# Kernel tuning notes

Hardware: AMD Instinct MI355X
Metric: run time of the kernel (lower is better)

Reference implementation:

```python
import jax, jax.numpy as jnp
import numpy as np

N = 100_000   # nodes
E = 1_600_000 # edges
G, H1, H2, Z = 64, 64, 64, 32


def _w(k, o, i):
    return jax.random.normal(k, (o, i), jnp.float32) * (1.0 / np.sqrt(i))


def setup_inputs() -> dict:
    key = jax.random.key(0)
    ks = jax.random.split(key, 16)
    inp = {
        "x": jax.random.normal(ks[0], (N, G), jnp.float32),
        "edge_src": jax.random.randint(ks[1], (E,), 0, N, jnp.int32),
        "edge_dst": jax.random.randint(ks[2], (E,), 0, N, jnp.int32),
        "eps": jax.random.normal(ks[3], (N, Z), jnp.float32),
        "W1": _w(ks[4], H1, G),  "b1": jnp.zeros((H1,), jnp.float32),
        "W2": _w(ks[5], H2, H1), "b2": jnp.zeros((H2,), jnp.float32),
        "W31": _w(ks[6], Z, H2), "b31": jnp.zeros((Z,), jnp.float32),
        "W32": _w(ks[7], Z, H2), "b32": jnp.zeros((Z,), jnp.float32),
        "W4": _w(ks[8], H2, Z),  "b4": jnp.zeros((H2,), jnp.float32),
        "W5": _w(ks[9], H1, H2), "b5": jnp.zeros((H1,), jnp.float32),
        "W6": _w(ks[10], G, H1), "b6": jnp.zeros((G,), jnp.float32),
    }
    return inp


def _gcn(h, W, b, act, src, dst, norm):
    # message: h_src * norm_src, gathered per edge  [E, d]
    m = (h * norm)[src]
    # reduce: sum over incoming edges, scaled by norm_dst  [N, d]
    agg = jax.ops.segment_sum(m, dst, num_segments=N) * norm
    # node apply: linear + activation
    return act(agg @ W.T + b)


def reference(x, edge_src, edge_dst, eps,
              W1, b1, W2, b2, W31, b31, W32, b32, W4, b4, W5, b5, W6, b6):
    # symmetric GCN norm: deg^{-1/2} from in-degree
    deg = jax.ops.segment_sum(jnp.ones((E,), jnp.float32), edge_dst, num_segments=N)
    norm = jax.lax.rsqrt(jnp.maximum(deg, 1.0))[:, None]  # [N,1]

    relu = jax.nn.relu
    ident = lambda h: h

    h = _gcn(x, W1, b1, relu, edge_src, edge_dst, norm)
    h = _gcn(h, W2, b2, relu, edge_src, edge_dst, norm)
    mu = _gcn(h, W31, b31, ident, edge_src, edge_dst, norm)
    log_var = _gcn(h, W32, b32, ident, edge_src, edge_dst, norm)

    z = eps * jnp.exp(0.5 * log_var) + mu

    h = _gcn(z, W4, b4, relu, edge_src, edge_dst, norm)
    h = _gcn(h, W5, b5, relu, edge_src, edge_dst, norm)
    recon = _gcn(h, W6, b6, jax.nn.sigmoid, edge_src, edge_dst, norm)
    return recon, mu, log_var
```

## Files before the change

kernel.cpp:

```cpp
#include <hip/hip_runtime.h>
#include <hip/hip_fp16.h>
#include <math.h>

#define NN 100000
#define NE 1600000
#define NBKT 391
#define CHUNK 8192
#define NB1 ((NE + CHUNK - 1) / CHUNK)

__global__ __launch_bounds__(256) void p0_hist_kernel(const int* __restrict__ dst,
                                                      int* __restrict__ bcnt) {
    __shared__ int h[NBKT];
    for (int b = threadIdx.x; b < NBKT; b += 256) h[b] = 0;
    __syncthreads();
    int e0 = blockIdx.x * CHUNK;
    for (int k = 0; k < CHUNK / 256; ++k) {
        int e = e0 + threadIdx.x + k * 256;
        if (e < NE) atomicAdd(&h[dst[e] >> 8], 1);
    }
    __syncthreads();
    for (int b = threadIdx.x; b < NBKT; b += 256)
        if (h[b]) atomicAdd(&bcnt[b], h[b]);
}

__global__ void scan_buckets_kernel(const int* __restrict__ bcnt, int* __restrict__ bbase,
                                    int* __restrict__ bcur) {
    __shared__ int s[512];
    int tid = threadIdx.x;
    int v = (tid < NBKT) ? bcnt[tid] : 0;
    s[tid] = v;
    __syncthreads();
    for (int off = 1; off < 512; off <<= 1) {
        int t = (tid >= off) ? s[tid - off] : 0;
        __syncthreads();
        s[tid] += t;
        __syncthreads();
    }
    if (tid < NBKT) { int ex = s[tid] - v; bbase[tid] = ex; bcur[tid] = ex; }
    if (tid == NBKT) bbase[NBKT] = NE;
}

__global__ __launch_bounds__(256) void p1_scatter_kernel(const int* __restrict__ src,
                                                         const int* __restrict__ dst,
                                                         int* __restrict__ bcur,
                                                         int2* __restrict__ gpair) {
    __shared__ int h[NBKT], rb[NBKT], hc[NBKT];
    int tid = threadIdx.x;
    for (int b = tid; b < NBKT; b += 256) { h[b] = 0; hc[b] = 0; }
    __syncthreads();
    int e0 = blockIdx.x * CHUNK;
    for (int k = 0; k < CHUNK / 256; ++k) {
        int e = e0 + tid + k * 256;
        if (e < NE) atomicAdd(&h[dst[e] >> 8], 1);
    }
    __syncthreads();
    for (int b = tid; b < NBKT; b += 256)
        rb[b] = h[b] ? atomicAdd(&bcur[b], h[b]) : 0;
    __syncthreads();
    for (int k = 0; k < CHUNK / 256; ++k) {
        int e = e0 + tid + k * 256;
        if (e < NE) {
            int d = dst[e], s = src[e];
            int b = d >> 8;
            int pos = rb[b] + atomicAdd(&hc[b], 1);
            gpair[pos] = make_int2(s, d);
        }
    }
}

__global__ __launch_bounds__(256) void p2_place_kernel(const int2* __restrict__ gpair,
                                                       const int* __restrict__ bbase,
                                                       int* __restrict__ csr,
                                                       int* __restrict__ row_start,
                                                       float* __restrict__ nrm) {
    __shared__ int cnt[256], nexcl[256], pcnt[256];
    int b = blockIdx.x, tid = threadIdx.x;
    int s0 = bbase[b], s1 = bbase[b + 1];
    cnt[tid] = 0; pcnt[tid] = 0;
    __syncthreads();
    for (int i = s0 + tid; i < s1; i += 256)
        atomicAdd(&cnt[gpair[i].y & 255], 1);
    __syncthreads();
    int v = cnt[tid];
    nexcl[tid] = v;
    __syncthreads();
    for (int off = 1; off < 256; off <<= 1) {
        int t = (tid >= off) ? nexcl[tid - off] : 0;
        __syncthreads();
        nexcl[tid] += t;
        __syncthreads();
    }
    int ex = nexcl[tid] - v;
    int node = (b << 8) + tid;
    if (node < NN) {
        row_start[node] = s0 + ex;
        nrm[node] = rsqrtf(fmaxf((float)v, 1.0f));
    }
    if (b == NBKT - 1 && tid == 0) row_start[NN] = NE;
    nexcl[tid] = s0 + ex;
    __syncthreads();
    for (int i = s0 + tid; i < s1; i += 256) {
        int2 p = gpair[i];
        int l = p.y & 255;
        int pos = nexcl[l] + atomicAdd(&pcnt[l], 1);
        csr[pos] = p.x;
    }
}

union H4 { uint2 u; __half2 h[2]; };

__global__ void scale_x_h_kernel(const float4* __restrict__ x4, const float* __restrict__ nrm,
                                 uint2* __restrict__ xs, int total4) {
    int i = blockIdx.x * blockDim.x + threadIdx.x;
    if (i < total4) {
        float nv = nrm[i >> 4];
        float4 v = x4[i];
        H4 w;
        w.h[0] = __floats2half2_rn(v.x * nv, v.y * nv);
        w.h[1] = __floats2half2_rn(v.z * nv, v.w * nv);
        xs[i] = w.u;
    }
}

template<int IN, int ACT, bool SCALE, bool DUAL>
__global__ __launch_bounds__(256) void gcn_fused_kernel(
        const __half* __restrict__ h,
        const float* __restrict__ nrm,
        const int* __restrict__ row_start,
        const int* __restrict__ csr,
        const float* __restrict__ Wa, const float* __restrict__ ba,
        const float* __restrict__ Wb, const float* __restrict__ bb,
        void* __restrict__ outv, float* __restrict__ out2,
        const float* __restrict__ eps, __half* __restrict__ zbuf) {
    __shared__ float Wt[64 * 65];
    __shared__ float bs[64];
    __shared__ __align__(16) float aggS[4][4][IN];

    int tid = threadIdx.x;
    if (DUAL) {
        for (int i = tid; i < 32 * 64; i += 256) {
            int o = i >> 6, k = i & 63;
            Wt[k * 65 + o]      = Wa[i];
            Wt[k * 65 + o + 32] = Wb[i];
        }
        if (tid < 32) { bs[tid] = ba[tid]; bs[tid + 32] = bb[tid]; }
    } else {
        for (int i = tid; i < 64 * IN; i += 256) {
            int o = i / IN, k = i % IN;
            Wt[k * 65 + o] = Wa[i];
        }
        if (tid < 64) bs[tid] = ba[tid];
    }
    __syncthreads();

    constexpr int RL  = IN / 4;
    constexpr int EPI = 64 / RL;
    int wave = tid >> 6, lane = tid & 63;
    int row_slot = lane / RL;
    int f4 = lane % RL;
    int nodeBase = (blockIdx.x * 4 + wave) * 4;

    const uint2* hp = (const uint2*)h;

    int rs[4], re[4];
#pragma unroll
    for (int i = 0; i < 4; ++i) {
        rs[i] = row_start[nodeBase + i];
        re[i] = row_start[nodeBase + i + 1];
    }
    int maxd = max(max(re[0] - rs[0], re[1] - rs[1]), max(re[2] - rs[2], re[3] - rs[3]));

    float4 acc[4];
#pragma unroll
    for (int i = 0; i < 4; ++i) acc[i] = make_float4(0.f, 0.f, 0.f, 0.f);

    for (int t = 0; t < maxd; t += EPI) {
#pragma unroll
        for (int i = 0; i < 4; ++i) {
            int jj = rs[i] + t + row_slot;
            bool ok = jj < re[i];
            int s = csr[ok ? jj : 0];
            float m = ok ? 1.f : 0.f;
            H4 v; v.u = hp[(size_t)s * RL + f4];
            float2 f01 = __half22float2(v.h[0]);
            float2 f23 = __half22float2(v.h[1]);
            acc[i].x = fmaf(m, f01.x, acc[i].x);
            acc[i].y = fmaf(m, f01.y, acc[i].y);
            acc[i].z = fmaf(m, f23.x, acc[i].z);
            acc[i].w = fmaf(m, f23.y, acc[i].w);
        }
    }

#pragma unroll
    for (int i = 0; i < 4; ++i) {
        for (int o = RL; o < 64; o <<= 1) {
            acc[i].x += __shfl_xor(acc[i].x, o);
            acc[i].y += __shfl_xor(acc[i].y, o);
            acc[i].z += __shfl_xor(acc[i].z, o);
            acc[i].w += __shfl_xor(acc[i].w, o);
        }
    }

    if (row_slot == 0) {
#pragma unroll
        for (int i = 0; i < 4; ++i)
            ((float4*)aggS[wave][i])[f4] = acc[i];
    }

#pragma unroll
    for (int i = 0; i < 4; ++i) {
        int node = nodeBase + i;
        float oa = 0.f;
#pragma unroll
        for (int k = 0; k < IN; ++k)
            oa = fmaf(aggS[wave][i][k], Wt[k * 65 + lane], oa);
        float nv = nrm[node];
        oa = oa * nv + bs[lane];
        if (ACT == 1) oa = fmaxf(oa, 0.f);
        if (ACT == 2) oa = 1.f / (1.f + expf(-oa));

        if (DUAL) {
            float* mu_p = (float*)outv;
            if (lane < 32) mu_p[(size_t)node * 32 + lane]        = oa;
            else           out2[(size_t)node * 32 + (lane - 32)] = oa;
            float lv_v = __shfl(oa, (lane + 32) & 63);
            if (lane < 32) {
                float e = eps[(size_t)node * 32 + lane];
                zbuf[(size_t)node * 32 + lane] = __float2half((e * expf(0.5f * lv_v) + oa) * nv);
            }
        } else if (SCALE) {
            ((__half*)outv)[(size_t)node * 64 + lane] = __float2half(oa * nv);
        } else {
            ((float*)outv)[(size_t)node * 64 + lane] = oa;
        }
    }
}

extern "C" void kernel_launch(void* const* d_in, const int* in_sizes, int n_in,
                              void* d_out, int out_size, void* d_ws, size_t ws_size,
                              hipStream_t stream) {
    const float* x    = (const float*)d_in[0];
    const int*   esrc = (const int*)d_in[1];
    const int*   edst = (const int*)d_in[2];
    const float* eps  = (const float*)d_in[3];
    const float* W1  = (const float*)d_in[4];  const float* b1  = (const float*)d_in[5];
    const float* W2  = (const float*)d_in[6];  const float* b2  = (const float*)d_in[7];
    const float* W31 = (const float*)d_in[8];  const float* b31 = (const float*)d_in[9];
    const float* W32 = (const float*)d_in[10]; const float* b32 = (const float*)d_in[11];
    const float* W4  = (const float*)d_in[12]; const float* b4  = (const float*)d_in[13];
    const float* W5  = (const float*)d_in[14]; const float* b5  = (const float*)d_in[15];
    const float* W6  = (const float*)d_in[16]; const float* b6  = (const float*)d_in[17];

    float* outp  = (float*)d_out;
    float* recon = outp;
    float* mu    = outp + (size_t)NN * 64;
    float* lv    = mu   + (size_t)NN * 32;

    int* wsI       = (int*)d_ws;
    int* bcnt      = wsI;
    int* bbase     = bcnt + 392;
    int* bcur      = bbase + 392;
    int* row_start = bcur + 392;
    int* csr       = row_start + NN + 4;
    float* nrm     = (float*)(csr + NE);
    __half* hA     = (__half*)(nrm + NN);
    __half* hB     = hA + (size_t)NN * 64;
    int2* gpair    = (int2*)hA;

    const int SB = 256;
    const int fgrid = NN / 16;

    hipMemsetAsync(bcnt, 0, 392 * sizeof(int), stream);
    p0_hist_kernel<<<NB1, 256, 0, stream>>>(edst, bcnt);
    scan_buckets_kernel<<<1, 512, 0, stream>>>(bcnt, bbase, bcur);
    p1_scatter_kernel<<<NB1, 256, 0, stream>>>(esrc, edst, bcur, gpair);
    p2_place_kernel<<<NBKT, 256, 0, stream>>>(gpair, bbase, csr, row_start, nrm);

    scale_x_h_kernel<<<(NN * 16 + SB - 1) / SB, SB, 0, stream>>>((const float4*)x, nrm, (uint2*)hA, NN * 16);

    gcn_fused_kernel<64, 1, true,  false><<<fgrid, 256, 0, stream>>>(hA, nrm, row_start, csr, W1,  b1,  nullptr, nullptr, hB,    nullptr, nullptr, nullptr);
    gcn_fused_kernel<64, 1, true,  false><<<fgrid, 256, 0, stream>>>(hB, nrm, row_start, csr, W2,  b2,  nullptr, nullptr, hA,    nullptr, nullptr, nullptr);
    gcn_fused_kernel<64, 0, false, true ><<<fgrid, 256, 0, stream>>>(hA, nrm, row_start, csr, W31, b31, W32,     b32,     mu,    lv,      eps,     hB);
    gcn_fused_kernel<32, 1, true,  false><<<fgrid, 256, 0, stream>>>(hB, nrm, row_start, csr, W4,  b4,  nullptr, nullptr, hA,    nullptr, nullptr, nullptr);
    gcn_fused_kernel<64, 1, true,  false><<<fgrid, 256, 0, stream>>>(hA, nrm, row_start, csr, W5,  b5,  nullptr, nullptr, hB,    nullptr, nullptr, nullptr);
    gcn_fused_kernel<64, 2, false, false><<<fgrid, 256, 0, stream>>>(hB, nrm, row_start, csr, W6,  b6,  nullptr, nullptr, recon, nullptr, nullptr, nullptr);
}
```

Baseline: 620.8 us.

## Pack edge pairs into one int and process 8 nodes per wave

The CSR build now packs each (src, dst-low-byte) pair into a single 32-bit int instead of an int2, halving the intermediate scatter traffic. The fused GCN kernel handles 8 nodes per wave instead of 4 and splits the gather loop into separate phases for index loads, feature loads and accumulation, so more independent loads are in flight. The grid is halved to match. The cost is more registers and possible lower occupancy, and a wave now loops to the maximum degree over 8 nodes, which adds masked work.

```diff
diff --git a/kernel.cpp b/kernel.cpp
--- a/kernel.cpp
+++ b/kernel.cpp
@@ -43,7 +43,7 @@
 __global__ __launch_bounds__(256) void p1_scatter_kernel(const int* __restrict__ src,
                                                          const int* __restrict__ dst,
                                                          int* __restrict__ bcur,
-                                                         int2* __restrict__ gpair) {
+                                                         int* __restrict__ gpair) {
     __shared__ int h[NBKT], rb[NBKT], hc[NBKT];
     int tid = threadIdx.x;
     for (int b = tid; b < NBKT; b += 256) { h[b] = 0; hc[b] = 0; }
@@ -63,12 +63,12 @@
             int d = dst[e], s = src[e];
             int b = d >> 8;
             int pos = rb[b] + atomicAdd(&hc[b], 1);
-            gpair[pos] = make_int2(s, d);
-        }
-    }
-}
-
-__global__ __launch_bounds__(256) void p2_place_kernel(const int2* __restrict__ gpair,
+            gpair[pos] = (s << 8) | (d & 255);
+        }
+    }
+}
+
+__global__ __launch_bounds__(256) void p2_place_kernel(const int* __restrict__ gpair,
                                                        const int* __restrict__ bbase,
                                                        int* __restrict__ csr,
                                                        int* __restrict__ row_start,
@@ -79,7 +79,7 @@
     cnt[tid] = 0; pcnt[tid] = 0;
     __syncthreads();
     for (int i = s0 + tid; i < s1; i += 256)
-        atomicAdd(&cnt[gpair[i].y & 255], 1);
+        atomicAdd(&cnt[gpair[i] & 255], 1);
     __syncthreads();
     int v = cnt[tid];
     nexcl[tid] = v;
@@ -100,10 +100,10 @@
     nexcl[tid] = s0 + ex;
     __syncthreads();
     for (int i = s0 + tid; i < s1; i += 256) {
-        int2 p = gpair[i];
-        int l = p.y & 255;
+        int p = gpair[i];
+        int l = p & 255;
         int pos = nexcl[l] + atomicAdd(&pcnt[l], 1);
-        csr[pos] = p.x;
+        csr[pos] = p >> 8;
     }
 }
 
@@ -132,9 +132,10 @@
         const float* __restrict__ Wb, const float* __restrict__ bb,
         void* __restrict__ outv, float* __restrict__ out2,
         const float* __restrict__ eps, __half* __restrict__ zbuf) {
+    constexpr int MLP = 8;
     __shared__ float Wt[64 * 65];
     __shared__ float bs[64];
-    __shared__ __align__(16) float aggS[4][4][IN];
+    __shared__ __align__(16) float aggS[4][MLP][IN];
 
     int tid = threadIdx.x;
     if (DUAL) {
@@ -158,41 +159,52 @@
     int wave = tid >> 6, lane = tid & 63;
     int row_slot = lane / RL;
     int f4 = lane % RL;
-    int nodeBase = (blockIdx.x * 4 + wave) * 4;
+    int nodeBase = (blockIdx.x * 4 + wave) * MLP;
 
     const uint2* hp = (const uint2*)h;
 
-    int rs[4], re[4];
-#pragma unroll
-    for (int i = 0; i < 4; ++i) {
-        rs[i] = row_start[nodeBase + i];
-        re[i] = row_start[nodeBase + i + 1];
-    }
-    int maxd = max(max(re[0] - rs[0], re[1] - rs[1]), max(re[2] - rs[2], re[3] - rs[3]));
-
-    float4 acc[4];
-#pragma unroll
-    for (int i = 0; i < 4; ++i) acc[i] = make_float4(0.f, 0.f, 0.f, 0.f);
+    int rsb[MLP], re[MLP];
+#pragma unroll
+    for (int i = 0; i < MLP; ++i) {
+        rsb[i] = row_start[nodeBase + i];
+        re[i]  = row_start[nodeBase + i + 1];
+    }
+    int maxd = 0;
+#pragma unroll
+    for (int i = 0; i < MLP; ++i) maxd = max(maxd, re[i] - rsb[i]);
+#pragma unroll
+    for (int i = 0; i < MLP; ++i) rsb[i] += row_slot;
+
+    float4 acc[MLP];
+#pragma unroll
+    for (int i = 0; i < MLP; ++i) acc[i] = make_float4(0.f, 0.f, 0.f, 0.f);
 
     for (int t = 0; t < maxd; t += EPI) {
-#pragma unroll
-        for (int i = 0; i < 4; ++i) {
-            int jj = rs[i] + t + row_slot;
+        int s[MLP]; float m[MLP];
+#pragma unroll
+        for (int i = 0; i < MLP; ++i) {
+            int jj = rsb[i] + t;
             bool ok = jj < re[i];
-            int s = csr[ok ? jj : 0];
-            float m = ok ? 1.f : 0.f;
-            H4 v; v.u = hp[(size_t)s * RL + f4];
-            float2 f01 = __half22float2(v.h[0]);
-            float2 f23 = __half22float2(v.h[1]);
-            acc[i].x = fmaf(m, f01.x, acc[i].x);
-            acc[i].y = fmaf(m, f01.y, acc[i].y);
-            acc[i].z = fmaf(m, f23.x, acc[i].z);
-            acc[i].w = fmaf(m, f23.y, acc[i].w);
-        }
-    }
-
-#pragma unroll
-    for (int i = 0; i < 4; ++i) {
+            s[i] = csr[ok ? jj : 0];
+            m[i] = ok ? 1.f : 0.f;
+        }
+        H4 v[MLP];
+#pragma unroll
+        for (int i = 0; i < MLP; ++i)
+            v[i].u = hp[(size_t)s[i] * RL + f4];
+#pragma unroll
+        for (int i = 0; i < MLP; ++i) {
+            float2 f01 = __half22float2(v[i].h[0]);
+            float2 f23 = __half22float2(v[i].h[1]);
+            acc[i].x = fmaf(m[i], f01.x, acc[i].x);
+            acc[i].y = fmaf(m[i], f01.y, acc[i].y);
+            acc[i].z = fmaf(m[i], f23.x, acc[i].z);
+            acc[i].w = fmaf(m[i], f23.y, acc[i].w);
+        }
+    }
+
+#pragma unroll
+    for (int i = 0; i < MLP; ++i) {
         for (int o = RL; o < 64; o <<= 1) {
             acc[i].x += __shfl_xor(acc[i].x, o);
             acc[i].y += __shfl_xor(acc[i].y, o);
@@ -203,12 +215,12 @@
 
     if (row_slot == 0) {
 #pragma unroll
-        for (int i = 0; i < 4; ++i)
+        for (int i = 0; i < MLP; ++i)
             ((float4*)aggS[wave][i])[f4] = acc[i];
     }
 
 #pragma unroll
-    for (int i = 0; i < 4; ++i) {
+    for (int i = 0; i < MLP; ++i) {
         int node = nodeBase + i;
         float oa = 0.f;
 #pragma unroll
@@ -265,10 +277,10 @@
     float* nrm     = (float*)(csr + NE);
     __half* hA     = (__half*)(nrm + NN);
     __half* hB     = hA + (size_t)NN * 64;
-    int2* gpair    = (int2*)hA;
+    int* gpair     = (int*)hA;
 
     const int SB = 256;
-    const int fgrid = NN / 16;
+    const int fgrid = NN / 32;
 
     hipMemsetAsync(bcnt, 0, 392 * sizeof(int), stream);
     p0_hist_kernel<<<NB1, 256, 0, stream>>>(edst, bcnt);
```

New measurement: 618.1 us. About the same (-0.4%).
